# Kernel tuning notes

Hardware: AMD Instinct MI355X
Metric: run time of the kernel (lower is better)

## Reference

```python
import jax, jax.numpy as jnp
from jax import lax
import numpy as np

B, C_IN, DIMS, NW = 8, 64, 64, 8
T, H, W = 16, 56, 56
HID = C_IN // 4 + 1
EPS = 1e-5


def setup_inputs() -> dict:
    key = jax.random.key(0)
    ks = jax.random.split(key, 8)
    fan_in = C_IN * 27
    x = jax.random.normal(ks[0], (B, C_IN, T, H, W), dtype=jnp.float32)
    weights = jax.random.normal(ks[1], (NW, DIMS, C_IN, 3, 3, 3), dtype=jnp.float32) * np.sqrt(2.0 / fan_in)
    biases = jax.random.normal(ks[2], (NW, DIMS), dtype=jnp.float32)
    W1 = jax.random.normal(ks[3], (HID, C_IN), dtype=jnp.float32) * np.sqrt(1.0 / C_IN)
    b1 = jnp.zeros((HID,), dtype=jnp.float32)
    W2 = jax.random.normal(ks[4], (NW, HID), dtype=jnp.float32) * np.sqrt(1.0 / HID)
    b2 = jnp.zeros((NW,), dtype=jnp.float32)
    gamma = jnp.ones((DIMS,), dtype=jnp.float32)
    beta = jnp.zeros((DIMS,), dtype=jnp.float32)
    return {"x": x, "weights": weights, "biases": biases, "W1": W1, "b1": b1,
            "W2": W2, "b2": b2, "gamma": gamma, "beta": beta, "epochs_num": 5}


def reference(x, weights, biases, W1, b1, W2, b2, gamma, beta, epochs_num):
    # temperature schedule (epochs_num is a Python int)
    tau = 30.0 - 2.9 * epochs_num if epochs_num < 10 else 1.0
    # global max pool over (T,H,W) -> (B, C_in); sum over singleton dims is identity
    pooled = jnp.max(x, axis=(2, 3, 4))
    h = jax.nn.relu(pooled @ W1.T + b1)
    logits = h @ W2.T + b2
    phi = jax.nn.softmax(logits / tau, axis=1)  # (B, NW)
    # synthesize per-sample kernels and biases
    dyn_w = jnp.einsum('bn,noidhw->boidhw', phi, weights)  # (B, DIMS, C_in, 3,3,3)
    dyn_b = phi @ biases  # (B, DIMS)
    # per-sample conv3d (equivalent to grouped conv with groups=B)
    def conv1(xi, wi):
        return lax.conv_general_dilated(
            xi[None], wi, window_strides=(1, 1, 1), padding='SAME',
            dimension_numbers=('NCDHW', 'OIDHW', 'NCDHW'))[0]
    y = jax.vmap(conv1)(x, dyn_w) + dyn_b[:, :, None, None, None]
    # BatchNorm3d (training mode: batch statistics, biased var) + ReLU
    mean = jnp.mean(y, axis=(0, 2, 3, 4))
    var = jnp.var(y, axis=(0, 2, 3, 4))
    yn = (y - mean[None, :, None, None, None]) * lax.rsqrt(var + EPS)[None, :, None, None, None]
    yn = yn * gamma[None, :, None, None, None] + beta[None, :, None, None, None]
    return jax.nn.relu(yn)
```

## Files before the change

### kernel.cpp

```cpp
#include <hip/hip_runtime.h>
#include <hip/hip_bf16.h>

#define B_   8
#define CIN  64
#define DIMS 64
#define NW   8
#define T_   16
#define H_   56
#define W_   56
#define HID  17
#define THW  (T_*H_*W_)
#define HW   (H_*W_)
#define NPC  401408
#define EPS  1e-5f
#define PROWS 348

typedef __bf16 bf16x8 __attribute__((ext_vector_type(8)));
typedef float f32x4 __attribute__((ext_vector_type(4)));

#define OFF_XT     0
#define OFF_AT     51380224
#define OFF_POOLED 53149696
#define OFF_CHSUM  53151744
#define OFF_CHSQ   53152000
#define OFF_PHI    53152256
#define OFF_DYNB   53152512
#define OFF_SCALE  53154560
#define OFF_SHIFT  53154816
#define OFF_Y      53155072
#define WS_NEED_BF16Y (OFF_Y + 51380224)

__device__ __forceinline__ unsigned short f2bf(float f) {
    unsigned int u = __float_as_uint(f);
    u += 0x7fffu + ((u >> 16) & 1u);
    return (unsigned short)(u >> 16);
}
__device__ __forceinline__ float bf2f(unsigned short u) {
    return __uint_as_float(((unsigned int)u) << 16);
}
__device__ __forceinline__ unsigned int fenc(float f) {
    unsigned int b = __float_as_uint(f);
    return (b & 0x80000000u) ? ~b : (b | 0x80000000u);
}
__device__ __forceinline__ float fdec(unsigned int e) {
    return (e & 0x80000000u) ? __uint_as_float(e & 0x7fffffffu) : __uint_as_float(~e);
}

__device__ __forceinline__ float waveRedSum(float v) {
    #pragma unroll
    for (int o = 32; o > 0; o >>= 1) v += __shfl_down(v, o);
    return v;
}

__global__ __launch_bounds__(256) void xpose_kernel(const float* __restrict__ x,
                                                    unsigned short* __restrict__ xT,
                                                    unsigned int* __restrict__ pooled_u) {
    __shared__ float tile[CIN * W_];
    const int h = blockIdx.x, t = blockIdx.y, b = blockIdx.z;
    const int tid = threadIdx.x;
    {
        const int w = tid & 63, cg = tid >> 6;
        if (w < W_) {
            const size_t base = ((size_t)(b * CIN) * T_ + t) * HW + h * W_ + w;
            #pragma unroll
            for (int k = 0; k < 16; ++k) {
                const int c = cg * 16 + k;
                tile[c * W_ + w] = x[base + (size_t)c * (T_ * HW)];
            }
        }
    }
    __syncthreads();
    {
        const int w = tid >> 2, cq = tid & 3;
        if (w < W_) {
            unsigned int pk[8];
            #pragma unroll
            for (int kk = 0; kk < 8; ++kk) {
                const float f0 = tile[(cq * 16 + kk * 2) * W_ + w];
                const float f1 = tile[(cq * 16 + kk * 2 + 1) * W_ + w];
                pk[kk] = (unsigned int)f2bf(f0) | ((unsigned int)f2bf(f1) << 16);
            }
            unsigned short* dst = xT + ((((size_t)b * T_ + t) * H_ + h) * W_ + w) * CIN + cq * 16;
            *reinterpret_cast<uint4*>(dst)     = make_uint4(pk[0], pk[1], pk[2], pk[3]);
            *reinterpret_cast<uint4*>(dst + 8) = make_uint4(pk[4], pk[5], pk[6], pk[7]);
        }
    }
    if (tid < CIN) {
        float m = -3.4e38f;
        #pragma unroll 8
        for (int w = 0; w < W_; ++w) m = fmaxf(m, tile[tid * W_ + w]);
        atomicMax(&pooled_u[b * CIN + tid], fenc(m));
    }
}

__global__ __launch_bounds__(256) void mlp_kernel(const unsigned int* __restrict__ pooled_u,
                                                  const float* __restrict__ W1,
                                                  const float* __restrict__ b1,
                                                  const float* __restrict__ W2,
                                                  const float* __restrict__ b2,
                                                  const float* __restrict__ biases,
                                                  const void* __restrict__ epochs,
                                                  float* __restrict__ phi_out,
                                                  float* __restrict__ dynb) {
    __shared__ float pool_s[B_ * CIN];
    __shared__ float h_s[B_ * HID];
    __shared__ float lg_s[B_ * NW];
    __shared__ float phi_s[B_ * NW];
    const int tid = threadIdx.x;
    for (int i = tid; i < B_ * CIN; i += 256) pool_s[i] = fdec(pooled_u[i]);
    __syncthreads();
    if (tid < B_ * HID) {
        const int bb = tid / HID, j = tid % HID;
        float acc = b1[j];
        #pragma unroll
        for (int c = 0; c < CIN; ++c) acc += pool_s[bb * CIN + c] * W1[j * CIN + c];
        h_s[tid] = fmaxf(acc, 0.0f);
    }
    __syncthreads();
    if (tid < B_ * NW) {
        const int bb = tid >> 3, n = tid & 7;
        float acc = b2[n];
        #pragma unroll
        for (int j = 0; j < HID; ++j) acc += h_s[bb * HID + j] * W2[n * HID + j];
        lg_s[tid] = acc;
    }
    __syncthreads();
    if (tid < B_) {
        int e = ((const int*)epochs)[0];
        if (e < 0 || e > 1000000) e = (int)(((const float*)epochs)[0]);
        const float tau = (e < 10) ? (30.0f - 2.9f * (float)e) : 1.0f;
        float mx = -3.4e38f;
        #pragma unroll
        for (int n = 0; n < NW; ++n) mx = fmaxf(mx, lg_s[tid * NW + n]);
        float ex[NW], s = 0.0f;
        #pragma unroll
        for (int n = 0; n < NW; ++n) { ex[n] = expf((lg_s[tid * NW + n] - mx) / tau); s += ex[n]; }
        const bool ok = (s >= 1.0f) && (s < 1e37f);
        const float inv = ok ? (1.0f / s) : 0.0f;
        #pragma unroll
        for (int n = 0; n < NW; ++n) phi_s[tid * NW + n] = ok ? (ex[n] * inv) : 0.125f;
    }
    __syncthreads();
    if (tid < B_ * NW) phi_out[tid] = phi_s[tid];
    for (int idx = tid; idx < B_ * DIMS; idx += 256) {
        const int bb = idx >> 6, o = idx & 63;
        float a = 0.0f;
        #pragma unroll
        for (int n = 0; n < NW; ++n) a += phi_s[bb * NW + n] * biases[n * DIMS + o];
        dynb[idx] = a;
    }
}

__global__ __launch_bounds__(256) void awgen_kernel(const float* __restrict__ weights,
                                                    const float* __restrict__ phi,
                                                    unsigned short* __restrict__ At2) {
    const int b = blockIdx.x >> 5, oc = blockIdx.x & 31;
    const int o0 = oc * 2;
    __shared__ float ph[NW];
    if (threadIdx.x < NW) ph[threadIdx.x] = phi[b * NW + threadIdx.x];
    __syncthreads();
    const float4* w4 = reinterpret_cast<const float4*>(weights);
    for (int j = threadIdx.x; j < 864; j += 256) {
        f32x4 a = (f32x4){0.f, 0.f, 0.f, 0.f};
        #pragma unroll
        for (int n = 0; n < NW; ++n) {
            const float4 wv = w4[(size_t)(n * 64 + o0) * 432 + j];
            a[0] += ph[n] * wv.x;
            a[1] += ph[n] * wv.y;
            a[2] += ph[n] * wv.z;
            a[3] += ph[n] * wv.w;
        }
        #pragma unroll
        for (int k = 0; k < 4; ++k) {
            const int idx = j * 4 + k;
            const int oo = idx / 1728;
            const int rem = idx - oo * 1728;
            const int i = rem / 27;
            const int tap = rem - i * 27;
            const int o = o0 + oo;
            const int m = o >> 4, colv = o & 15;
            const int ks = i >> 5, kgv = (i >> 3) & 3, jj = i & 7;
            const size_t dst = (size_t)(b * 27 + tap) * 4096
                             + ((((ks * 4 + m) * 64) + kgv * 16 + colv) * 8 + jj);
            At2[dst] = f2bf(a[k]);
        }
    }
}

template<int BF16Y>
__global__ __launch_bounds__(256) void conv_kernel(const unsigned short* __restrict__ xT,
                                                   const unsigned short* __restrict__ At2,
                                                   const float* __restrict__ dynb,
                                                   float* __restrict__ yf,
                                                   unsigned short* __restrict__ yb) {
    __shared__ __align__(16) unsigned char xs[PROWS * 128];
    const int swz = (blockIdx.x & 7) * 224 + (blockIdx.x >> 3);
    const int b = swz / 224;
    const int rem = swz - b * 224;
    const int t = rem / 14, hg = rem - t * 14;
    const int tid = threadIdx.x;
    const int wave = tid >> 6, lane = tid & 63;
    const int col = lane & 15, kg = lane >> 4;
    const int hr = wave;
    const int h = hg * 4 + hr;

    for (int idx = tid; idx < PROWS * 8; idx += 256) {
        const int p = idx >> 3;
        const int hh = p / 58, ww = p - hh * 58;
        const int hha = hg * 4 + hh - 1;
        if (hha < 0 || hha >= H_ || ww == 0 || ww == 57)
            *reinterpret_cast<uint4*>(&xs[idx * 16]) = make_uint4(0u, 0u, 0u, 0u);
    }

    f32x4 acc[4][4];
    #pragma unroll
    for (int m = 0; m < 4; ++m)
        #pragma unroll
        for (int n = 0; n < 4; ++n) acc[m][n] = (f32x4){0.f, 0.f, 0.f, 0.f};

    const int sub = lane >> 3, q = lane & 7;

    for (int kd = 0; kd < 3; ++kd) {
        const int td = t + kd - 1;
        if (td < 0 || td >= T_) continue;
        __syncthreads();
        for (int item = wave; item < 42; item += 4) {
            const int hh = item / 7, qv = item - hh * 7;
            const int hha = hg * 4 + hh - 1;
            if (hha < 0 || hha >= H_) continue;
            const int p0 = hh * 58 + 1 + qv * 8;
            const int p = p0 + sub;
            const int w = qv * 8 + sub;
            const int qq = q ^ (p & 7);
            const unsigned short* src = xT
                + ((((size_t)b * T_ + td) * H_ + hha) * W_ + w) * CIN + qq * 8;
            __builtin_amdgcn_global_load_lds(
                (const __attribute__((address_space(1))) unsigned int*)(const void*)src,
                (__attribute__((address_space(3))) unsigned int*)(void*)&xs[p0 * 128],
                16, 0, 0);
        }
        asm volatile("s_waitcnt vmcnt(0)" ::: "memory");
        __syncthreads();
        __builtin_amdgcn_s_setprio(1);
        #pragma unroll
        for (int kh = 0; kh < 3; ++kh) {
            #pragma unroll
            for (int kw = 0; kw < 3; ++kw) {
                const int tap = kd * 9 + kh * 3 + kw;
                const unsigned short* ap = At2 + (size_t)(b * 27 + tap) * 4096;
                bf16x8 afr[4][2], bfr[4][2];
                #pragma unroll
                for (int ks = 0; ks < 2; ++ks)
                    #pragma unroll
                    for (int m = 0; m < 4; ++m)
                        afr[m][ks] = *reinterpret_cast<const bf16x8*>(
                            ap + (((ks * 4 + m) * 64) + lane) * 8);
                #pragma unroll
                for (int n = 0; n < 4; ++n) {
                    int ww = n * 16 + col + kw;
                    if (ww > 57) ww = 57;
                    const int p = (hr + kh) * 58 + ww;
                    #pragma unroll
                    for (int ks = 0; ks < 2; ++ks) {
                        const int slot = (ks * 4 + kg) ^ (p & 7);
                        bfr[n][ks] = *reinterpret_cast<const bf16x8*>(&xs[p * 128 + slot * 16]);
                    }
                }
                #pragma unroll
                for (int ks = 0; ks < 2; ++ks)
                    #pragma unroll
                    for (int m = 0; m < 4; ++m)
                        #pragma unroll
                        for (int n = 0; n < 4; ++n)
                            acc[m][n] = __builtin_amdgcn_mfma_f32_16x16x32_bf16(
                                afr[m][ks], bfr[n][ks], acc[m][n], 0, 0, 0);
            }
        }
        __builtin_amdgcn_s_setprio(0);
    }

    #pragma unroll
    for (int m = 0; m < 4; ++m) {
        #pragma unroll
        for (int r = 0; r < 4; ++r) {
            const int o = m * 16 + kg * 4 + r;
            const float db = dynb[b * DIMS + o];
            const size_t base = ((size_t)(b * DIMS + o) * T_ + t) * HW + h * W_;
            #pragma unroll
            for (int n = 0; n < 4; ++n) {
                const int w = n * 16 + col;
                if (w < W_) {
                    const float v = acc[m][n][r] + db;
                    if (BF16Y) yb[base + w] = f2bf(v);
                    else       yf[base + w] = v;
                }
            }
        }
    }
}

__global__ __launch_bounds__(256) void stats_f32_kernel(const float* __restrict__ y,
                                                        float* __restrict__ chsum,
                                                        float* __restrict__ chsq) {
    const int bo = blockIdx.x;
    const int o = bo & 63;
    const float4* src = reinterpret_cast<const float4*>(y + (size_t)bo * THW);
    float s = 0.0f, qq = 0.0f;
    for (int idx = threadIdx.x; idx < THW / 4; idx += 256) {
        float4 v = src[idx];
        s += v.x + v.y + v.z + v.w;
        qq += v.x * v.x + v.y * v.y + v.z * v.z + v.w * v.w;
    }
    s = waveRedSum(s);
    qq = waveRedSum(qq);
    __shared__ float ls[4], lq[4];
    const int wave = threadIdx.x >> 6, lane = threadIdx.x & 63;
    if (lane == 0) { ls[wave] = s; lq[wave] = qq; }
    __syncthreads();
    if (threadIdx.x == 0) {
        atomicAdd(&chsum[o], ls[0] + ls[1] + ls[2] + ls[3]);
        atomicAdd(&chsq[o],  lq[0] + lq[1] + lq[2] + lq[3]);
    }
}

__global__ __launch_bounds__(256) void stats_bf16_kernel(const unsigned short* __restrict__ yb,
                                                         float* __restrict__ chsum,
                                                         float* __restrict__ chsq) {
    const int bo = blockIdx.x;
    const int o = bo & 63;
    const uint4* src = reinterpret_cast<const uint4*>(yb + (size_t)bo * THW);
    float s = 0.0f, qq = 0.0f;
    for (int idx = threadIdx.x; idx < THW / 8; idx += 256) {
        uint4 v = src[idx];
        unsigned int vv[4] = {v.x, v.y, v.z, v.w};
        #pragma unroll
        for (int k = 0; k < 4; ++k) {
            float f0 = __uint_as_float((vv[k] & 0xffffu) << 16);
            float f1 = __uint_as_float(vv[k] & 0xffff0000u);
            s += f0 + f1;
            qq += f0 * f0 + f1 * f1;
        }
    }
    s = waveRedSum(s);
    qq = waveRedSum(qq);
    __shared__ float ls[4], lq[4];
    const int wave = threadIdx.x >> 6, lane = threadIdx.x & 63;
    if (lane == 0) { ls[wave] = s; lq[wave] = qq; }
    __syncthreads();
    if (threadIdx.x == 0) {
        atomicAdd(&chsum[o], ls[0] + ls[1] + ls[2] + ls[3]);
        atomicAdd(&chsq[o],  lq[0] + lq[1] + lq[2] + lq[3]);
    }
}

__global__ void fin_kernel(const float* __restrict__ chsum, const float* __restrict__ chsq,
                           const float* __restrict__ gamma, const float* __restrict__ beta,
                           float* __restrict__ scale, float* __restrict__ shift,
                           const unsigned int* __restrict__ pooled_u,
                           const float* __restrict__ phi,
                           int hostflags, float* __restrict__ out) {
    const int o = threadIdx.x;
    if (o < DIMS) {
        const float inv = 1.0f / (float)NPC;
        const float mean = chsum[o] * inv;
        const float var = chsq[o] * inv - mean * mean;
        const bool ok = (fabsf(mean) < 1e30f) && (var >= 0.0f) && (var < 1e30f);
        const float rstd = ok ? rsqrtf(var + EPS) : 0.0f;
        const float s = gamma[o] * rstd;
        scale[o] = ok ? s : 0.0f;
        shift[o] = ok ? (beta[o] - mean * s) : 0.69f;
    }
    if (o == 0) {
        int D = 32;
        const float p0 = fdec(pooled_u[0]);
        if (isfinite(p0) && fabsf(p0) > 1e-20f) D += 16;
        float sp = 0.0f, mp = 0.0f;
        for (int n = 0; n < NW; ++n) { sp += phi[n]; mp = fmaxf(mp, phi[n]); }
        if (fabsf(sp - 1.0f) < 0.01f) D += 32;
        float sq = 0.0f;
        for (int c = 0; c < DIMS; ++c) sq += chsq[c];
        if (sq > 1e-10f) D += 128;
        if (mp > 0.25f) D += 256;
        D += hostflags;
        if (D != 32 + 16 + 32 + 128) out[0] = (float)D;
    }
}

__global__ __launch_bounds__(256) void norm_f32_kernel(float* __restrict__ y,
                                                       const float* __restrict__ scale,
                                                       const float* __restrict__ shift) {
    const int bo = blockIdx.x >> 2, qq = blockIdx.x & 3;
    const int o = bo & 63;
    const float s = scale[o], sh = shift[o];
    float4* buf = reinterpret_cast<float4*>(y + (size_t)bo * THW) + qq * (THW / 16);
    for (int idx = threadIdx.x; idx < THW / 16; idx += 256) {
        float4 v = buf[idx];
        v.x = fmaxf(v.x * s + sh, 0.0f);
        v.y = fmaxf(v.y * s + sh, 0.0f);
        v.z = fmaxf(v.z * s + sh, 0.0f);
        v.w = fmaxf(v.w * s + sh, 0.0f);
        buf[idx] = v;
    }
}

__global__ __launch_bounds__(256) void norm_bf16_kernel(const unsigned short* __restrict__ yb,
                                                        const float* __restrict__ scale,
                                                        const float* __restrict__ shift,
                                                        float* __restrict__ out) {
    const int bo = blockIdx.x >> 2, qq = blockIdx.x & 3;
    const int o = bo & 63;
    const float s = scale[o], sh = shift[o];
    const uint4* src = reinterpret_cast<const uint4*>(yb + (size_t)bo * THW) + qq * (THW / 32);
    float4* dst = reinterpret_cast<float4*>(out + (size_t)bo * THW) + qq * (THW / 16);
    for (int idx = threadIdx.x; idx < THW / 32; idx += 256) {
        uint4 v = src[idx];
        unsigned int vv[4] = {v.x, v.y, v.z, v.w};
        float4 r0, r1;
        float* rp[2] = {&r0.x, &r1.x};
        #pragma unroll
        for (int k = 0; k < 4; ++k) {
            float f0 = __uint_as_float((vv[k] & 0xffffu) << 16);
            float f1 = __uint_as_float(vv[k] & 0xffff0000u);
            rp[k >> 1][(k & 1) * 2]     = fmaxf(f0 * s + sh, 0.0f);
            rp[k >> 1][(k & 1) * 2 + 1] = fmaxf(f1 * s + sh, 0.0f);
        }
        dst[idx * 2]     = r0;
        dst[idx * 2 + 1] = r1;
    }
}

extern "C" void kernel_launch(void* const* d_in, const int* in_sizes, int n_in,
                              void* d_out, int out_size, void* d_ws, size_t ws_size,
                              hipStream_t stream) {
    const float* x       = (const float*)d_in[0];
    const float* weights = (const float*)d_in[1];
    const float* biases  = (const float*)d_in[2];
    const float* W1      = (const float*)d_in[3];
    const float* b1      = (const float*)d_in[4];
    const float* W2      = (const float*)d_in[5];
    const float* b2      = (const float*)d_in[6];
    const float* gamma   = (const float*)d_in[7];
    const float* beta    = (const float*)d_in[8];
    const void*  epochs  = (const void*)d_in[9];

    float* out = (float*)d_out;
    char* ws = (char*)d_ws;
    unsigned short* xT   = (unsigned short*)(ws + OFF_XT);
    unsigned short* At2  = (unsigned short*)(ws + OFF_AT);
    unsigned int* pooled = (unsigned int*)(ws + OFF_POOLED);
    float* chsum  = (float*)(ws + OFF_CHSUM);
    float* chsq   = (float*)(ws + OFF_CHSQ);
    float* phi    = (float*)(ws + OFF_PHI);
    float* dynb   = (float*)(ws + OFF_DYNB);
    float* scale  = (float*)(ws + OFF_SCALE);
    float* shift  = (float*)(ws + OFF_SHIFT);
    unsigned short* ybf  = (unsigned short*)(ws + OFF_Y);

    const bool bf16y = (ws_size >= (size_t)WS_NEED_BF16Y);

    int hflags = 0;
    {
        const int expect[10] = {25690112, 884736, 512, 1088, 17, 136, 8, 64, 64, 1};
        if (n_in != 10) hflags |= 512;
        else {
            for (int i = 0; i < 10; ++i)
                if (in_sizes[i] != expect[i]) { hflags |= 512; break; }
        }
        if (out_size != 25690112) hflags |= 1024;
        if (ws_size < 53155072) hflags |= 2048;
    }

    hipMemsetAsync(ws + OFF_POOLED, 0, 2560, stream);

    xpose_kernel<<<dim3(H_, T_, B_), 256, 0, stream>>>(x, xT, pooled);
    mlp_kernel<<<1, 256, 0, stream>>>(pooled, W1, b1, W2, b2, biases, epochs, phi, dynb);
    awgen_kernel<<<256, 256, 0, stream>>>(weights, phi, At2);
    if (bf16y) {
        conv_kernel<1><<<1792, 256, 0, stream>>>(xT, At2, dynb, out, ybf);
        stats_bf16_kernel<<<B_ * DIMS, 256, 0, stream>>>(ybf, chsum, chsq);
        fin_kernel<<<1, 64, 0, stream>>>(chsum, chsq, gamma, beta, scale, shift,
                                         pooled, phi, hflags, out);
        norm_bf16_kernel<<<2048, 256, 0, stream>>>(ybf, scale, shift, out);
    } else {
        conv_kernel<0><<<1792, 256, 0, stream>>>(xT, At2, dynb, out, nullptr);
        stats_f32_kernel<<<B_ * DIMS, 256, 0, stream>>>(out, chsum, chsq);
        fin_kernel<<<1, 64, 0, stream>>>(chsum, chsq, gamma, beta, scale, shift,
                                         pooled, phi, hflags, out);
        norm_f32_kernel<<<2048, 256, 0, stream>>>(out, scale, shift);
    }
}
```

Baseline: 233.3 us.

## Fold MLP into awgen and BN finalize into norm kernels, narrow setprio

Removes the single-block MLP kernel by having each awgen block recompute its sample's hidden layer, logits and softmax locally. It also removes the finalize kernel by computing per-channel scale and shift inside each norm block. The debug/diagnostic flag logic that could overwrite out[0] is dropped. The conv's priority raise now wraps only the MFMA section per tap. The goal is to cut two tiny serial kernel launches and their gaps, at the cost of redundant small computations per block.

Result: faster. 220.1 us (-5.7%).

```diff
diff --git a/kernel.cpp b/kernel.cpp
--- a/kernel.cpp
+++ b/kernel.cpp
@@ -23,10 +23,7 @@
 #define OFF_POOLED 53149696
 #define OFF_CHSUM  53151744
 #define OFF_CHSQ   53152000
-#define OFF_PHI    53152256
 #define OFF_DYNB   53152512
-#define OFF_SCALE  53154560
-#define OFF_SHIFT  53154816
 #define OFF_Y      53155072
 #define WS_NEED_BF16Y (OFF_Y + 51380224)
 
@@ -93,74 +90,59 @@
     }
 }
 
-__global__ __launch_bounds__(256) void mlp_kernel(const unsigned int* __restrict__ pooled_u,
-                                                  const float* __restrict__ W1,
-                                                  const float* __restrict__ b1,
-                                                  const float* __restrict__ W2,
-                                                  const float* __restrict__ b2,
-                                                  const float* __restrict__ biases,
-                                                  const void* __restrict__ epochs,
-                                                  float* __restrict__ phi_out,
-                                                  float* __restrict__ dynb) {
-    __shared__ float pool_s[B_ * CIN];
-    __shared__ float h_s[B_ * HID];
-    __shared__ float lg_s[B_ * NW];
-    __shared__ float phi_s[B_ * NW];
+__global__ __launch_bounds__(256) void awgen_kernel(const float* __restrict__ weights,
+                                                    const unsigned int* __restrict__ pooled_u,
+                                                    const float* __restrict__ W1,
+                                                    const float* __restrict__ b1,
+                                                    const float* __restrict__ W2,
+                                                    const float* __restrict__ b2,
+                                                    const float* __restrict__ biases,
+                                                    const void* __restrict__ epochs,
+                                                    float* __restrict__ dynb,
+                                                    unsigned short* __restrict__ At2) {
+    const int b = blockIdx.x >> 5, oc = blockIdx.x & 31;
+    const int o0 = oc * 2;
+    __shared__ float ph[NW];
+    __shared__ float h_s[HID];
     const int tid = threadIdx.x;
-    for (int i = tid; i < B_ * CIN; i += 256) pool_s[i] = fdec(pooled_u[i]);
-    __syncthreads();
-    if (tid < B_ * HID) {
-        const int bb = tid / HID, j = tid % HID;
-        float acc = b1[j];
-        #pragma unroll
-        for (int c = 0; c < CIN; ++c) acc += pool_s[bb * CIN + c] * W1[j * CIN + c];
+    if (tid < HID) {
+        float acc = b1[tid];
+        #pragma unroll
+        for (int c = 0; c < CIN; ++c) acc += fdec(pooled_u[b * CIN + c]) * W1[tid * CIN + c];
         h_s[tid] = fmaxf(acc, 0.0f);
     }
     __syncthreads();
-    if (tid < B_ * NW) {
-        const int bb = tid >> 3, n = tid & 7;
-        float acc = b2[n];
-        #pragma unroll
-        for (int j = 0; j < HID; ++j) acc += h_s[bb * HID + j] * W2[n * HID + j];
-        lg_s[tid] = acc;
-    }
-    __syncthreads();
-    if (tid < B_) {
+    if (tid < NW) {
+        float acc = b2[tid];
+        #pragma unroll
+        for (int j = 0; j < HID; ++j) acc += h_s[j] * W2[tid * HID + j];
+        ph[tid] = acc;
+    }
+    __syncthreads();
+    if (tid == 0) {
         int e = ((const int*)epochs)[0];
         if (e < 0 || e > 1000000) e = (int)(((const float*)epochs)[0]);
         const float tau = (e < 10) ? (30.0f - 2.9f * (float)e) : 1.0f;
         float mx = -3.4e38f;
         #pragma unroll
-        for (int n = 0; n < NW; ++n) mx = fmaxf(mx, lg_s[tid * NW + n]);
+        for (int n = 0; n < NW; ++n) mx = fmaxf(mx, ph[n]);
         float ex[NW], s = 0.0f;
         #pragma unroll
-        for (int n = 0; n < NW; ++n) { ex[n] = expf((lg_s[tid * NW + n] - mx) / tau); s += ex[n]; }
+        for (int n = 0; n < NW; ++n) { ex[n] = expf((ph[n] - mx) / tau); s += ex[n]; }
         const bool ok = (s >= 1.0f) && (s < 1e37f);
         const float inv = ok ? (1.0f / s) : 0.0f;
         #pragma unroll
-        for (int n = 0; n < NW; ++n) phi_s[tid * NW + n] = ok ? (ex[n] * inv) : 0.125f;
-    }
-    __syncthreads();
-    if (tid < B_ * NW) phi_out[tid] = phi_s[tid];
-    for (int idx = tid; idx < B_ * DIMS; idx += 256) {
-        const int bb = idx >> 6, o = idx & 63;
+        for (int n = 0; n < NW; ++n) ph[n] = ok ? (ex[n] * inv) : 0.125f;
+    }
+    __syncthreads();
+    if (oc == 0 && tid < DIMS) {
         float a = 0.0f;
         #pragma unroll
-        for (int n = 0; n < NW; ++n) a += phi_s[bb * NW + n] * biases[n * DIMS + o];
-        dynb[idx] = a;
-    }
-}
-
-__global__ __launch_bounds__(256) void awgen_kernel(const float* __restrict__ weights,
-                                                    const float* __restrict__ phi,
-                                                    unsigned short* __restrict__ At2) {
-    const int b = blockIdx.x >> 5, oc = blockIdx.x & 31;
-    const int o0 = oc * 2;
-    __shared__ float ph[NW];
-    if (threadIdx.x < NW) ph[threadIdx.x] = phi[b * NW + threadIdx.x];
-    __syncthreads();
+        for (int n = 0; n < NW; ++n) a += ph[n] * biases[n * DIMS + tid];
+        dynb[b * DIMS + tid] = a;
+    }
     const float4* w4 = reinterpret_cast<const float4*>(weights);
-    for (int j = threadIdx.x; j < 864; j += 256) {
+    for (int j = tid; j < 864; j += 256) {
         f32x4 a = (f32x4){0.f, 0.f, 0.f, 0.f};
         #pragma unroll
         for (int n = 0; n < NW; ++n) {
@@ -241,7 +223,6 @@
         }
         asm volatile("s_waitcnt vmcnt(0)" ::: "memory");
         __syncthreads();
-        __builtin_amdgcn_s_setprio(1);
         #pragma unroll
         for (int kh = 0; kh < 3; ++kh) {
             #pragma unroll
@@ -266,6 +247,7 @@
                         bfr[n][ks] = *reinterpret_cast<const bf16x8*>(&xs[p * 128 + slot * 16]);
                     }
                 }
+                __builtin_amdgcn_s_setprio(1);
                 #pragma unroll
                 for (int ks = 0; ks < 2; ++ks)
                     #pragma unroll
@@ -274,9 +256,9 @@
                         for (int n = 0; n < 4; ++n)
                             acc[m][n] = __builtin_amdgcn_mfma_f32_16x16x32_bf16(
                                 afr[m][ks], bfr[n][ks], acc[m][n], 0, 0, 0);
+                __builtin_amdgcn_s_setprio(0);
             }
         }
-        __builtin_amdgcn_s_setprio(0);
     }
 
     #pragma unroll
@@ -353,45 +335,20 @@
     }
 }
 
-__global__ void fin_kernel(const float* __restrict__ chsum, const float* __restrict__ chsq,
-                           const float* __restrict__ gamma, const float* __restrict__ beta,
-                           float* __restrict__ scale, float* __restrict__ shift,
-                           const unsigned int* __restrict__ pooled_u,
-                           const float* __restrict__ phi,
-                           int hostflags, float* __restrict__ out) {
-    const int o = threadIdx.x;
-    if (o < DIMS) {
-        const float inv = 1.0f / (float)NPC;
-        const float mean = chsum[o] * inv;
-        const float var = chsq[o] * inv - mean * mean;
-        const bool ok = (fabsf(mean) < 1e30f) && (var >= 0.0f) && (var < 1e30f);
-        const float rstd = ok ? rsqrtf(var + EPS) : 0.0f;
-        const float s = gamma[o] * rstd;
-        scale[o] = ok ? s : 0.0f;
-        shift[o] = ok ? (beta[o] - mean * s) : 0.69f;
-    }
-    if (o == 0) {
-        int D = 32;
-        const float p0 = fdec(pooled_u[0]);
-        if (isfinite(p0) && fabsf(p0) > 1e-20f) D += 16;
-        float sp = 0.0f, mp = 0.0f;
-        for (int n = 0; n < NW; ++n) { sp += phi[n]; mp = fmaxf(mp, phi[n]); }
-        if (fabsf(sp - 1.0f) < 0.01f) D += 32;
-        float sq = 0.0f;
-        for (int c = 0; c < DIMS; ++c) sq += chsq[c];
-        if (sq > 1e-10f) D += 128;
-        if (mp > 0.25f) D += 256;
-        D += hostflags;
-        if (D != 32 + 16 + 32 + 128) out[0] = (float)D;
-    }
-}
-
 __global__ __launch_bounds__(256) void norm_f32_kernel(float* __restrict__ y,
-                                                       const float* __restrict__ scale,
-                                                       const float* __restrict__ shift) {
+                                                       const float* __restrict__ chsum,
+                                                       const float* __restrict__ chsq,
+                                                       const float* __restrict__ gamma,
+                                                       const float* __restrict__ beta) {
     const int bo = blockIdx.x >> 2, qq = blockIdx.x & 3;
     const int o = bo & 63;
-    const float s = scale[o], sh = shift[o];
+    const float inv = 1.0f / (float)NPC;
+    const float mean = chsum[o] * inv;
+    const float var = chsq[o] * inv - mean * mean;
+    const bool ok = (fabsf(mean) < 1e30f) && (var >= 0.0f) && (var < 1e30f);
+    const float rstd = ok ? rsqrtf(var + EPS) : 0.0f;
+    const float s = gamma[o] * rstd;
+    const float sh = ok ? (beta[o] - mean * s) : 0.69f;
     float4* buf = reinterpret_cast<float4*>(y + (size_t)bo * THW) + qq * (THW / 16);
     for (int idx = threadIdx.x; idx < THW / 16; idx += 256) {
         float4 v = buf[idx];
@@ -404,12 +361,20 @@
 }
 
 __global__ __launch_bounds__(256) void norm_bf16_kernel(const unsigned short* __restrict__ yb,
-                                                        const float* __restrict__ scale,
-                                                        const float* __restrict__ shift,
+                                                        const float* __restrict__ chsum,
+                                                        const float* __restrict__ chsq,
+                                                        const float* __restrict__ gamma,
+                                                        const float* __restrict__ beta,
                                                         float* __restrict__ out) {
     const int bo = blockIdx.x >> 2, qq = blockIdx.x & 3;
     const int o = bo & 63;
-    const float s = scale[o], sh = shift[o];
+    const float inv = 1.0f / (float)NPC;
+    const float mean = chsum[o] * inv;
+    const float var = chsq[o] * inv - mean * mean;
+    const bool ok = (fabsf(mean) < 1e30f) && (var >= 0.0f) && (var < 1e30f);
+    const float rstd = ok ? rsqrtf(var + EPS) : 0.0f;
+    const float s = gamma[o] * rstd;
+    const float sh = ok ? (beta[o] - mean * s) : 0.69f;
     const uint4* src = reinterpret_cast<const uint4*>(yb + (size_t)bo * THW) + qq * (THW / 32);
     float4* dst = reinterpret_cast<float4*>(out + (size_t)bo * THW) + qq * (THW / 16);
     for (int idx = threadIdx.x; idx < THW / 32; idx += 256) {
@@ -450,42 +415,23 @@
     unsigned int* pooled = (unsigned int*)(ws + OFF_POOLED);
     float* chsum  = (float*)(ws + OFF_CHSUM);
     float* chsq   = (float*)(ws + OFF_CHSQ);
-    float* phi    = (float*)(ws + OFF_PHI);
     float* dynb   = (float*)(ws + OFF_DYNB);
-    float* scale  = (float*)(ws + OFF_SCALE);
-    float* shift  = (float*)(ws + OFF_SHIFT);
     unsigned short* ybf  = (unsigned short*)(ws + OFF_Y);
 
     const bool bf16y = (ws_size >= (size_t)WS_NEED_BF16Y);
 
-    int hflags = 0;
-    {
-        const int expect[10] = {25690112, 884736, 512, 1088, 17, 136, 8, 64, 64, 1};
-        if (n_in != 10) hflags |= 512;
-        else {
-            for (int i = 0; i < 10; ++i)
-                if (in_sizes[i] != expect[i]) { hflags |= 512; break; }
-        }
-        if (out_size != 25690112) hflags |= 1024;
-        if (ws_size < 53155072) hflags |= 2048;
-    }
-
     hipMemsetAsync(ws + OFF_POOLED, 0, 2560, stream);
 
     xpose_kernel<<<dim3(H_, T_, B_), 256, 0, stream>>>(x, xT, pooled);
-    mlp_kernel<<<1, 256, 0, stream>>>(pooled, W1, b1, W2, b2, biases, epochs, phi, dynb);
-    awgen_kernel<<<256, 256, 0, stream>>>(weights, phi, At2);
+    awgen_kernel<<<256, 256, 0, stream>>>(weights, pooled, W1, b1, W2, b2,
+                                          biases, epochs, dynb, At2);
     if (bf16y) {
         conv_kernel<1><<<1792, 256, 0, stream>>>(xT, At2, dynb, out, ybf);
         stats_bf16_kernel<<<B_ * DIMS, 256, 0, stream>>>(ybf, chsum, chsq);
-        fin_kernel<<<1, 64, 0, stream>>>(chsum, chsq, gamma, beta, scale, shift,
-                                         pooled, phi, hflags, out);
-        norm_bf16_kernel<<<2048, 256, 0, stream>>>(ybf, scale, shift, out);
+        norm_bf16_kernel<<<2048, 256, 0, stream>>>(ybf, chsum, chsq, gamma, beta, out);
     } else {
         conv_kernel<0><<<1792, 256, 0, stream>>>(xT, At2, dynb, out, nullptr);
         stats_f32_kernel<<<B_ * DIMS, 256, 0, stream>>>(out, chsum, chsq);
-        fin_kernel<<<1, 64, 0, stream>>>(chsum, chsq, gamma, beta, scale, shift,
-                                         pooled, phi, hflags, out);
-        norm_f32_kernel<<<2048, 256, 0, stream>>>(out, scale, shift);
-    }
-}
+        norm_f32_kernel<<<2048, 256, 0, stream>>>(out, chsum, chsq, gamma, beta);
+    }
+}
```
